# Kernel optimization log

Hardware: AMD Instinct MI355X
Metric: run time of the kernel (lower is better)

Reference implementation:

```python
import jax, jax.numpy as jnp
import numpy as np

D_MODEL = 2048
EXPAND = 2
INNER = EXPAND * D_MODEL          # 4096
HEADDIM = 64
NHEADS = INNER // HEADDIM         # 64
D_CONV = 4
BATCH, SEQLEN = 2, 4096


def setup_inputs() -> dict:
    key = jax.random.key(0)
    ks = jax.random.split(key, 12)
    f32 = jnp.float32
    return {
        "hidden_states": jax.random.normal(ks[0], (BATCH, SEQLEN, D_MODEL), f32),
        "in_proj_w": jax.random.normal(ks[1], (INNER, D_MODEL), f32) * 0.02,
        "gate_proj_w": jax.random.normal(ks[2], (INNER, D_MODEL), f32) * 0.02,
        "out_proj_w": jax.random.normal(ks[3], (D_MODEL, INNER), f32) * 0.02,
        "conv_weight": jax.random.normal(ks[4], (INNER, D_CONV), f32) * 0.02,
        "conv_bias": jnp.zeros((INNER,), f32),
        "dt_w": jax.random.normal(ks[5], (NHEADS, HEADDIM), f32) * 0.02,
        "dt_b": jnp.zeros((NHEADS,), f32),
        "A_log": jax.random.normal(ks[6], (NHEADS, HEADDIM), f32) * 0.1,
        "B": jax.random.normal(ks[7], (NHEADS, HEADDIM), f32) * 0.02,
        "C": jax.random.normal(ks[8], (NHEADS, HEADDIM), f32) * 0.02,
        "D": jnp.ones((NHEADS, HEADDIM), f32),
    }


def _dw_causal_conv_silu(x, w, b):
    # x: (B, L, C), w: (C, K), b: (C,). Causal depthwise conv + SiLU.
    K = w.shape[1]
    L = x.shape[1]
    xp = jnp.pad(x, ((0, 0), (K - 1, 0), (0, 0)))
    y = b
    for k in range(K):  # K=4, tiny fixed loop
        y = y + w[:, k] * xp[:, k:k + L, :]
    return jax.nn.silu(y)


def _diag_ssm_scan(a, u):
    # Linear recurrence s_t = a_t * s_{t-1} + u_t along axis=1 (seqlen).
    def comb(c1, c2):
        a1, b1 = c1
        a2, b2 = c2
        return a1 * a2, a2 * b1 + b2
    _, s = jax.lax.associative_scan(comb, (a, u), axis=1)
    return s


def reference(hidden_states, in_proj_w, gate_proj_w, out_proj_w,
              conv_weight, conv_bias, dt_w, dt_b, A_log, B, C, D):
    batch, seqlen, _ = hidden_states.shape
    projected = jnp.einsum('bld,cd->blc', hidden_states, in_proj_w)
    conv_out = _dw_causal_conv_silu(projected, conv_weight, conv_bias)
    gate = jax.nn.sigmoid(jnp.einsum('bld,cd->blc', hidden_states, gate_proj_w))

    X = conv_out.reshape(batch, seqlen, NHEADS, HEADDIM)
    dt = jax.nn.softplus(jnp.einsum('blhp,hp->blh', X, dt_w) + dt_b)  # (b,l,h)
    A = -jnp.exp(A_log)                                               # (h,p)

    a = jnp.exp(dt[..., None] * A)          # (b,l,h,p) decay factors
    u = dt[..., None] * B * X               # (b,l,h,p) driven input
    s = _diag_ssm_scan(a, u)                # (b,l,h,p) states
    y = C * s + D * X                       # (b,l,h,p)

    combined = y.reshape(batch, seqlen, INNER) * gate
    return jnp.einsum('blc,dc->bld', combined, out_proj_w)
```

## Files before the change

kernel.cpp:

```cpp
#include <hip/hip_runtime.h>
#include <cstdint>
#include <cstddef>

typedef unsigned short ushort;
typedef __attribute__((ext_vector_type(8))) short short8;
typedef __attribute__((ext_vector_type(8))) unsigned short ushort8;
typedef __attribute__((ext_vector_type(4))) float float4v;

#define DM    2048
#define INNERC 4096
#define LSEQ  4096
#define NBATCH 2
#define MROWS 8192
#define NHH   64
#define HDD   64
#define NCHUNK 32
#define CHLEN  128
#define CROWS 8

__device__ __forceinline__ float bf2f(ushort u) {
    return __uint_as_float(((unsigned int)u) << 16);
}
__device__ __forceinline__ ushort f2bf(float f) {
    unsigned int u = __float_as_uint(f);
    unsigned int r = u + 0x7FFFu + ((u >> 16) & 1u);
    return (ushort)(r >> 16);
}

__device__ __forceinline__ void async_cp16(const ushort* __restrict__ g, ushort* l) {
    __builtin_amdgcn_global_load_lds(
        (const __attribute__((address_space(1))) unsigned int*)g,
        (__attribute__((address_space(3))) unsigned int*)l,
        16, 0, 0);
}

__global__ void diag_kernel(float* __restrict__ out, float val) {
    if (threadIdx.x == 0 && blockIdx.x == 0) out[0] = val;
}

__global__ __launch_bounds__(256) void cast_bf16_kernel(
    const float* __restrict__ in, ushort* __restrict__ out, int n) {
    const int i = (blockIdx.x * 256 + threadIdx.x) * 8;
    if (i + 8 > n) return;
    const float4v a = *(const float4v*)(in + i);
    const float4v b = *(const float4v*)(in + i + 4);
    ushort8 o;
    o[0] = f2bf(a[0]); o[1] = f2bf(a[1]); o[2] = f2bf(a[2]); o[3] = f2bf(a[3]);
    o[4] = f2bf(b[0]); o[5] = f2bf(b[1]); o[6] = f2bf(b[2]); o[7] = f2bf(b[3]);
    *(ushort8*)(out + i) = o;
}


#define PHASE_PRE() do { \
    __builtin_amdgcn_sched_barrier(0); \
    __builtin_amdgcn_s_barrier(); \
    asm volatile("s_waitcnt lgkmcnt(0)" ::: "memory"); \
    __builtin_amdgcn_sched_barrier(0); } while (0)

#define PHASE_POST() do { \
    __builtin_amdgcn_sched_barrier(0); \
    __builtin_amdgcn_s_barrier(); } while (0)

#define MFMA_Q(RL, CL) do { \
    __builtin_amdgcn_s_setprio(1); \
    _Pragma("unroll") for (int rm = 0; rm < 4; ++rm) \
    _Pragma("unroll") for (int cn = 0; cn < 2; ++cn) \
    _Pragma("unroll") for (int kk = 0; kk < 2; ++kk) \
        acc[(RL) + rm][(CL) + cn] = __builtin_amdgcn_mfma_f32_16x16x32_bf16( \
            af[(RL) + rm][kk], bf[(CL) + cn][kk], acc[(RL) + rm][(CL) + cn], 0, 0, 0); \
    __builtin_amdgcn_s_setprio(0); } while (0)

#define READ_B2(BUF, CNLO) do { \
    _Pragma("unroll") for (int cn = 0; cn < 2; ++cn) \
    _Pragma("unroll") for (int kk = 0; kk < 2; ++kk) { \
        const int rB = wn * 64 + ((CNLO) + cn) * 16 + l15; \
        bf[(CNLO) + cn][kk] = *(const short8*)&Bs[BUF][ \
            (rB * 8 + ((kk * 4 + l4) ^ swz7)) * 8]; \
    } } while (0)

template <int EPI>
__global__ __launch_bounds__(512, 2) void gemm256(
    const ushort* __restrict__ Ab, const ushort* __restrict__ Wb,
    void* __restrict__ Out, const ushort* __restrict__ Aux,
    int M, int N, int K) {
    __shared__ ushort As[2][16384];
    __shared__ ushort Bs[2][16384];

    const int tid  = threadIdx.x;
    const int lane = tid & 63;
    const int w    = tid >> 6;
    const int wm   = w >> 2;
    const int wn   = w & 3;
    const int l15  = lane & 15;
    const int l4   = lane >> 4;
    const int swz7 = l15 & 7;

    const int gx   = gridDim.x;
    const int nwg  = gx * gridDim.y;
    const int orig = blockIdx.y * gx + blockIdx.x;
    const int swz  = (orig & 7) * (nwg >> 3) + (orig >> 3);
    const int row0 = (swz / gx) * 256;
    const int col0 = (swz % gx) * 256;

    const int ni = K >> 7;

    float4v acc[8][4];
#pragma unroll
    for (int i2 = 0; i2 < 8; i2++)
#pragma unroll
        for (int j2 = 0; j2 < 4; j2++) {
            float4v z = {0.f, 0.f, 0.f, 0.f};
            acc[i2][j2] = z;
        }

    short8 af[8][2], bf[4][2];

    auto stage = [&](const ushort* __restrict__ G, int grow0, int t, ushort* dst) {
#pragma unroll
        for (int j = 0; j < 2; ++j) {
            const int c  = j * 512 + tid;
            const int r  = c >> 3;
            const int kg = (c & 7) ^ (r & 7);
            async_cp16(G + (size_t)(grow0 + r) * K + (t << 6) + kg * 8, dst + c * 8);
        }
    };

    auto readAall = [&](int b) {
#pragma unroll
        for (int rm = 0; rm < 8; ++rm)
#pragma unroll
            for (int kk = 0; kk < 2; ++kk) {
                const int rA = wm * 128 + rm * 16 + l15;
                af[rm][kk] = *(const short8*)&As[b][
                    (rA * 8 + ((kk * 4 + l4) ^ swz7)) * 8];
            }
    };

    stage(Ab, row0,       0, &As[0][0]);
    stage(Ab, row0 + 128, 0, &As[0][8192]);
    stage(Wb, col0,       0, &Bs[0][0]);
    stage(Wb, col0 + 128, 0, &Bs[0][8192]);
    stage(Ab, row0,       1, &As[1][0]);
    stage(Ab, row0 + 128, 1, &As[1][8192]);
    stage(Wb, col0,       1, &Bs[1][0]);
    asm volatile("s_waitcnt vmcnt(6)" ::: "memory");
    __builtin_amdgcn_s_barrier();

#pragma unroll 1
    for (int i = 0; i < ni; ++i) {
        const int u = 2 * i;
        const bool last = (i == ni - 1);

        readAall(0);
        READ_B2(0, 0);
        stage(Wb, col0 + 128, u + 1, &Bs[1][8192]);
        PHASE_PRE();
        MFMA_Q(0, 0);
        PHASE_POST();

        READ_B2(0, 2);
        if (!last) stage(Ab, row0, u + 2, &As[0][0]);
        PHASE_PRE();
        MFMA_Q(0, 2);
        PHASE_POST();

        if (!last) stage(Ab, row0 + 128, u + 2, &As[0][8192]);
        PHASE_PRE();
        MFMA_Q(4, 2);
        PHASE_POST();

        if (!last) stage(Wb, col0, u + 2, &Bs[0][0]);
        PHASE_PRE();
        MFMA_Q(4, 0);
        __builtin_amdgcn_sched_barrier(0);
        if (last) { asm volatile("s_waitcnt vmcnt(0)" ::: "memory"); }
        else      { asm volatile("s_waitcnt vmcnt(6)" ::: "memory"); }
        __builtin_amdgcn_s_barrier();

        readAall(1);
        READ_B2(1, 0);
        if (!last) stage(Wb, col0 + 128, u + 2, &Bs[0][8192]);
        PHASE_PRE();
        MFMA_Q(0, 0);
        PHASE_POST();

        READ_B2(1, 2);
        if (!last) stage(Ab, row0, u + 3, &As[1][0]);
        PHASE_PRE();
        MFMA_Q(0, 2);
        PHASE_POST();

        if (!last) stage(Ab, row0 + 128, u + 3, &As[1][8192]);
        PHASE_PRE();
        MFMA_Q(4, 2);
        PHASE_POST();

        if (!last) stage(Wb, col0, u + 3, &Bs[1][0]);
        PHASE_PRE();
        MFMA_Q(4, 0);
        __builtin_amdgcn_sched_barrier(0);
        if (!last) { asm volatile("s_waitcnt vmcnt(6)" ::: "memory"); }
        __builtin_amdgcn_s_barrier();
    }

#pragma unroll
    for (int rm = 0; rm < 8; ++rm) {
#pragma unroll
        for (int cn = 0; cn < 4; ++cn) {
            const int r0 = row0 + wm * 128 + rm * 16 + l4 * 4;
            const int cc = col0 + wn * 64 + cn * 16 + l15;
#pragma unroll
            for (int rr = 0; rr < 4; ++rr) {
                const float v = acc[rm][cn][rr];
                const size_t off = (size_t)(r0 + rr) * N + cc;
                if (EPI == 0) {
                    ((ushort*)Out)[off] = f2bf(v);
                } else if (EPI == 1) {
                    const float g = 1.0f / (1.0f + __expf(-v));
                    ((ushort*)Out)[off] = f2bf(g * bf2f(Aux[off]));
                } else {
                    ((float*)Out)[off] = v;
                }
            }
        }
    }
}

__global__ __launch_bounds__(256) void conv_silu_kernel(
    const ushort* __restrict__ proj, const float* __restrict__ cw,
    const float* __restrict__ cb, ushort* __restrict__ X) {
    const int blk  = blockIdx.x;
    const int half = blk & 1;
    const int tile = blk >> 1;
    const int bl0  = tile * CROWS;
    const bool atStart = ((bl0 & (LSEQ - 1)) == 0);
    const int c0 = half * 2048 + threadIdx.x * 8;

    float4v w[8];
    const float4v* wp4 = (const float4v*)(cw + (size_t)c0 * 4);
#pragma unroll
    for (int t = 0; t < 8; t++) w[t] = wp4[t];
    float bias[8];
    const float4v b0 = *(const float4v*)(cb + c0);
    const float4v b1 = *(const float4v*)(cb + c0 + 4);
#pragma unroll
    for (int t = 0; t < 4; t++) { bias[t] = b0[t]; bias[t + 4] = b1[t]; }

    const size_t base = (size_t)bl0 * INNERC + c0;
    ushort8 w0, w1, w2;
    const ushort8 zz = {0, 0, 0, 0, 0, 0, 0, 0};
    if (atStart) {
        w0 = zz; w1 = zz; w2 = zz;
    } else {
        w0 = *(const ushort8*)(proj + base - 3 * (size_t)INNERC);
        w1 = *(const ushort8*)(proj + base - 2 * (size_t)INNERC);
        w2 = *(const ushort8*)(proj + base - 1 * (size_t)INNERC);
    }
#pragma unroll
    for (int r = 0; r < CROWS; r++) {
        const ushort8 cur = *(const ushort8*)(proj + base + (size_t)r * INNERC);
        ushort8 o;
#pragma unroll
        for (int j = 0; j < 8; j++) {
            const float acc = bias[j]
                + w[j][0] * bf2f(w0[j]) + w[j][1] * bf2f(w1[j])
                + w[j][2] * bf2f(w2[j]) + w[j][3] * bf2f(cur[j]);
            o[j] = f2bf(acc / (1.0f + __expf(-acc)));
        }
        *(ushort8*)(X + base + (size_t)r * INNERC) = o;
        w0 = w1; w1 = w2; w2 = cur;
    }
}

__global__ __launch_bounds__(64) void dt_kernel(
    const ushort* __restrict__ X, const float* __restrict__ dtw,
    const float* __restrict__ dtb, float* __restrict__ dt) {
    const int bl = blockIdx.x;
    const int h  = threadIdx.x;
    const ushort* xp = X + (size_t)bl * INNERC + h * 64;
    const float*  wp = dtw + h * 64;
    float acc = 0.0f;
#pragma unroll
    for (int p0 = 0; p0 < 64; p0 += 8) {
        const ushort8 xv = *(const ushort8*)(xp + p0);
#pragma unroll
        for (int j = 0; j < 8; j++) acc += bf2f(xv[j]) * wp[p0 + j];
    }
    const float z = acc + dtb[h];
    dt[bl * 64 + h] = (z > 20.0f) ? z : __logf(1.0f + __expf(z));
}

__global__ __launch_bounds__(256) void scan_pass1(
    const ushort* __restrict__ X, const float* __restrict__ dt,
    const float* __restrict__ A_log, const float* __restrict__ Bv,
    float* __restrict__ sumP, float* __restrict__ sumS) {
    const int task = blockIdx.x * 4 + (threadIdx.x >> 6);
    const int p  = threadIdx.x & 63;
    const int ch = task & (NCHUNK - 1);
    const int bh = task >> 5;
    const int h  = bh & 63;
    const int b  = bh >> 6;
    const float Ac = -__expf(A_log[h * 64 + p]);
    const float Bc = Bv[h * 64 + p];
    float Pr = 1.0f, s = 0.0f;
    const int bl0 = b * LSEQ + ch * CHLEN;
#pragma unroll 4
    for (int i = 0; i < CHLEN; i++) {
        const int bl   = bl0 + i;
        const float dtv = dt[bl * 64 + h];
        const float x   = bf2f(X[(size_t)bl * INNERC + h * 64 + p]);
        const float a   = __expf(dtv * Ac);
        Pr *= a;
        s = a * s + dtv * Bc * x;
    }
    sumP[(size_t)task * 64 + p] = Pr;
    sumS[(size_t)task * 64 + p] = s;
}

__global__ __launch_bounds__(64) void scan_pass2(
    const float* __restrict__ sumP, const float* __restrict__ sumS,
    float* __restrict__ carry) {
    const int bh = blockIdx.x;
    const int p  = threadIdx.x;
    float c = 0.0f;
    for (int ch = 0; ch < NCHUNK; ch++) {
        const size_t idx = ((size_t)bh * NCHUNK + ch) * 64 + p;
        carry[idx] = c;
        c = sumP[idx] * c + sumS[idx];
    }
}

__global__ __launch_bounds__(256) void scan_pass3(
    const ushort* __restrict__ X, const float* __restrict__ dt,
    const float* __restrict__ carry,
    const float* __restrict__ A_log, const float* __restrict__ Bv,
    const float* __restrict__ Cv, const float* __restrict__ Dv,
    ushort* __restrict__ Y) {
    const int task = blockIdx.x * 4 + (threadIdx.x >> 6);
    const int p  = threadIdx.x & 63;
    const int ch = task & (NCHUNK - 1);
    const int bh = task >> 5;
    const int h  = bh & 63;
    const int b  = bh >> 6;
    const float Ac = -__expf(A_log[h * 64 + p]);
    const float Bc = Bv[h * 64 + p];
    const float Cc = Cv[h * 64 + p];
    const float Dc = Dv[h * 64 + p];
    float s = carry[(size_t)task * 64 + p];
    const int bl0 = b * LSEQ + ch * CHLEN;
#pragma unroll 2
    for (int i = 0; i < CHLEN; i++) {
        const int bl = bl0 + i;
        const size_t xoff = (size_t)bl * INNERC + h * 64 + p;
        const float dtv = dt[bl * 64 + h];
        const float x   = bf2f(X[xoff]);
        const float a   = __expf(dtv * Ac);
        s = a * s + dtv * Bc * x;
        Y[xoff] = f2bf(Cc * s + Dc * x);
    }
}

#define OFF_PROJ  ((size_t)0)
#define OFF_HID   ((size_t)67108864)
#define OFF_WB    ((size_t)100663296)
#define OFF_DT    ((size_t)117440512)
#define OFF_SUMP  ((size_t)119537664)
#define OFF_SUMS  ((size_t)120586240)
#define OFF_CARRY ((size_t)121634816)
#define WS_NEEDED ((size_t)122683392)

extern "C" void kernel_launch(void* const* d_in, const int* in_sizes, int n_in,
                              void* d_out, int out_size, void* d_ws, size_t ws_size,
                              hipStream_t stream) {
    if (ws_size < WS_NEEDED) {
        diag_kernel<<<1, 64, 0, stream>>>((float*)d_out, (float)(ws_size >> 20));
        return;
    }
    const float* hidden = (const float*)d_in[0];
    const float* w_in   = (const float*)d_in[1];
    const float* w_gate = (const float*)d_in[2];
    const float* w_out  = (const float*)d_in[3];
    const float* conv_w = (const float*)d_in[4];
    const float* conv_b = (const float*)d_in[5];
    const float* dt_w   = (const float*)d_in[6];
    const float* dt_b   = (const float*)d_in[7];
    const float* A_log  = (const float*)d_in[8];
    const float* Bv     = (const float*)d_in[9];
    const float* Cv     = (const float*)d_in[10];
    const float* Dv     = (const float*)d_in[11];

    char* ws = (char*)d_ws;
    ushort* projbuf = (ushort*)(ws + OFF_PROJ);
    ushort* hid16   = (ushort*)(ws + OFF_HID);
    ushort* wbuf    = (ushort*)(ws + OFF_WB);
    float*  dtf     = (float*)(ws + OFF_DT);
    float*  sumP    = (float*)(ws + OFF_SUMP);
    float*  sumS    = (float*)(ws + OFF_SUMS);
    float*  carry   = (float*)(ws + OFF_CARRY);
    ushort* x16     = (ushort*)d_out;

    cast_bf16_kernel<<<8192, 256, 0, stream>>>(hidden, hid16, MROWS * DM);
    cast_bf16_kernel<<<4096, 256, 0, stream>>>(w_in, wbuf, INNERC * DM);

    gemm256<0><<<dim3(INNERC / 256, MROWS / 256), 512, 0, stream>>>(
        hid16, wbuf, projbuf, nullptr, MROWS, INNERC, DM);

    conv_silu_kernel<<<(MROWS / CROWS) * 2, 256, 0, stream>>>(projbuf, conv_w, conv_b, x16);
    dt_kernel<<<MROWS, 64, 0, stream>>>(x16, dt_w, dt_b, dtf);

    scan_pass1<<<(NBATCH * NHH * NCHUNK) / 4, 256, 0, stream>>>(
        x16, dtf, A_log, Bv, sumP, sumS);
    scan_pass2<<<NBATCH * NHH, 64, 0, stream>>>(sumP, sumS, carry);
    scan_pass3<<<(NBATCH * NHH * NCHUNK) / 4, 256, 0, stream>>>(
        x16, dtf, carry, A_log, Bv, Cv, Dv, projbuf);

    cast_bf16_kernel<<<4096, 256, 0, stream>>>(w_gate, wbuf, INNERC * DM);
    gemm256<1><<<dim3(INNERC / 256, MROWS / 256), 512, 0, stream>>>(
        hid16, wbuf, projbuf, projbuf, MROWS, INNERC, DM);

    cast_bf16_kernel<<<4096, 256, 0, stream>>>(w_out, wbuf, DM * INNERC);
    gemm256<2><<<dim3(DM / 256, MROWS / 256), 512, 0, stream>>>(
        projbuf, wbuf, d_out, nullptr, MROWS, DM, INNERC);
}
```

Before: 778.7 us.

## Split A-fragment LDS reads into halves and reorder async staging schedule

Replaces the single 8-row A-fragment register array with two 4-row halves loaded just before their MFMA quadrants, which cuts register pressure and spreads LDS reads across phases. Reorders which global-to-LDS async copies are issued in each phase, prefetching more B in the prologue, and adjusts the vmcnt and lgkmcnt waits to match. It also drops the sched_barrier fences and the memory clobbers on lgkmcnt waits, giving the compiler more freedom to schedule. The risks are hazards from the looser waits and new buffer-reuse ordering (for example, writing As[1] in the same iteration it is read), plus scheduling that is less predictable without the barriers.

New measurement: 683.4 us. -12.2%, faster.

```diff
diff --git a/kernel.cpp b/kernel.cpp
--- a/kernel.cpp
+++ b/kernel.cpp
@@ -51,24 +51,29 @@
 }
 
 
-#define PHASE_PRE() do { \
-    __builtin_amdgcn_sched_barrier(0); \
+#define PH_PRE() do { \
     __builtin_amdgcn_s_barrier(); \
-    asm volatile("s_waitcnt lgkmcnt(0)" ::: "memory"); \
-    __builtin_amdgcn_sched_barrier(0); } while (0)
-
-#define PHASE_POST() do { \
-    __builtin_amdgcn_sched_barrier(0); \
+    asm volatile("s_waitcnt lgkmcnt(0)"); } while (0)
+
+#define PH_POST() do { \
     __builtin_amdgcn_s_barrier(); } while (0)
 
-#define MFMA_Q(RL, CL) do { \
+#define MFMA_Q(AF, RBASE, CL) do { \
     __builtin_amdgcn_s_setprio(1); \
     _Pragma("unroll") for (int rm = 0; rm < 4; ++rm) \
     _Pragma("unroll") for (int cn = 0; cn < 2; ++cn) \
     _Pragma("unroll") for (int kk = 0; kk < 2; ++kk) \
-        acc[(RL) + rm][(CL) + cn] = __builtin_amdgcn_mfma_f32_16x16x32_bf16( \
-            af[(RL) + rm][kk], bf[(CL) + cn][kk], acc[(RL) + rm][(CL) + cn], 0, 0, 0); \
+        acc[(RBASE) + rm][(CL) + cn] = __builtin_amdgcn_mfma_f32_16x16x32_bf16( \
+            AF[rm][kk], bf[(CL) + cn][kk], acc[(RBASE) + rm][(CL) + cn], 0, 0, 0); \
     __builtin_amdgcn_s_setprio(0); } while (0)
+
+#define READ_A(DST, BUF, HB) do { \
+    _Pragma("unroll") for (int rm = 0; rm < 4; ++rm) \
+    _Pragma("unroll") for (int kk = 0; kk < 2; ++kk) { \
+        const int rA = wm * 128 + (HB) * 64 + rm * 16 + l15; \
+        DST[rm][kk] = *(const short8*)&As[BUF][ \
+            (rA * 8 + ((kk * 4 + l4) ^ swz7)) * 8]; \
+    } } while (0)
 
 #define READ_B2(BUF, CNLO) do { \
     _Pragma("unroll") for (int cn = 0; cn < 2; ++cn) \
@@ -113,7 +118,7 @@
             acc[i2][j2] = z;
         }
 
-    short8 af[8][2], bf[4][2];
+    short8 afL[4][2], afH[4][2], bf[4][2];
 
     auto stage = [&](const ushort* __restrict__ G, int grow0, int t, ushort* dst) {
 #pragma unroll
@@ -123,17 +128,6 @@
             const int kg = (c & 7) ^ (r & 7);
             async_cp16(G + (size_t)(grow0 + r) * K + (t << 6) + kg * 8, dst + c * 8);
         }
-    };
-
-    auto readAall = [&](int b) {
-#pragma unroll
-        for (int rm = 0; rm < 8; ++rm)
-#pragma unroll
-            for (int kk = 0; kk < 2; ++kk) {
-                const int rA = wm * 128 + rm * 16 + l15;
-                af[rm][kk] = *(const short8*)&As[b][
-                    (rA * 8 + ((kk * 4 + l4) ^ swz7)) * 8];
-            }
     };
 
     stage(Ab, row0,       0, &As[0][0]);
@@ -143,7 +137,8 @@
     stage(Ab, row0,       1, &As[1][0]);
     stage(Ab, row0 + 128, 1, &As[1][8192]);
     stage(Wb, col0,       1, &Bs[1][0]);
-    asm volatile("s_waitcnt vmcnt(6)" ::: "memory");
+    stage(Wb, col0 + 128, 1, &Bs[1][8192]);
+    asm volatile("s_waitcnt vmcnt(8)" ::: "memory");
     __builtin_amdgcn_s_barrier();
 
 #pragma unroll 1
@@ -151,55 +146,61 @@
         const int u = 2 * i;
         const bool last = (i == ni - 1);
 
-        readAall(0);
+        READ_A(afL, 0, 0);
         READ_B2(0, 0);
-        stage(Wb, col0 + 128, u + 1, &Bs[1][8192]);
-        PHASE_PRE();
-        MFMA_Q(0, 0);
-        PHASE_POST();
+        asm volatile("s_waitcnt lgkmcnt(8)");
+        PH_PRE();
+        MFMA_Q(afL, 0, 0);
+        PH_POST();
 
         READ_B2(0, 2);
+        PH_PRE();
+        MFMA_Q(afL, 0, 2);
+        PH_POST();
+
+        READ_A(afH, 0, 1);
+        if (!last) stage(Wb, col0, u + 2, &Bs[0][0]);
+        PH_PRE();
+        MFMA_Q(afH, 4, 2);
+        PH_POST();
+
+        if (!last) stage(Wb, col0 + 128, u + 2, &Bs[0][8192]);
+        PH_PRE();
+        MFMA_Q(afH, 4, 0);
+        if (last) { asm volatile("s_waitcnt vmcnt(0)" ::: "memory"); }
+        else      { asm volatile("s_waitcnt vmcnt(4)" ::: "memory"); }
+        __builtin_amdgcn_s_barrier();
+
+        READ_A(afL, 1, 0);
+        READ_B2(1, 0);
         if (!last) stage(Ab, row0, u + 2, &As[0][0]);
-        PHASE_PRE();
-        MFMA_Q(0, 2);
-        PHASE_POST();
-
+        asm volatile("s_waitcnt lgkmcnt(8)");
+        PH_PRE();
+        MFMA_Q(afL, 0, 0);
+        PH_POST();
+
+        READ_B2(1, 2);
         if (!last) stage(Ab, row0 + 128, u + 2, &As[0][8192]);
-        PHASE_PRE();
-        MFMA_Q(4, 2);
-        PHASE_POST();
-
-        if (!last) stage(Wb, col0, u + 2, &Bs[0][0]);
-        PHASE_PRE();
-        MFMA_Q(4, 0);
-        __builtin_amdgcn_sched_barrier(0);
-        if (last) { asm volatile("s_waitcnt vmcnt(0)" ::: "memory"); }
-        else      { asm volatile("s_waitcnt vmcnt(6)" ::: "memory"); }
-        __builtin_amdgcn_s_barrier();
-
-        readAall(1);
-        READ_B2(1, 0);
-        if (!last) stage(Wb, col0 + 128, u + 2, &Bs[0][8192]);
-        PHASE_PRE();
-        MFMA_Q(0, 0);
-        PHASE_POST();
-
-        READ_B2(1, 2);
-        if (!last) stage(Ab, row0, u + 3, &As[1][0]);
-        PHASE_PRE();
-        MFMA_Q(0, 2);
-        PHASE_POST();
-
-        if (!last) stage(Ab, row0 + 128, u + 3, &As[1][8192]);
-        PHASE_PRE();
-        MFMA_Q(4, 2);
-        PHASE_POST();
-
-        if (!last) stage(Wb, col0, u + 3, &Bs[1][0]);
-        PHASE_PRE();
-        MFMA_Q(4, 0);
-        __builtin_amdgcn_sched_barrier(0);
-        if (!last) { asm volatile("s_waitcnt vmcnt(6)" ::: "memory"); }
+        PH_PRE();
+        MFMA_Q(afL, 0, 2);
+        PH_POST();
+
+        READ_A(afH, 1, 1);
+        if (!last) {
+            stage(Wb, col0,       u + 3, &Bs[1][0]);
+            stage(Wb, col0 + 128, u + 3, &Bs[1][8192]);
+        }
+        PH_PRE();
+        MFMA_Q(afH, 4, 2);
+        PH_POST();
+
+        if (!last) {
+            stage(Ab, row0,       u + 3, &As[1][0]);
+            stage(Ab, row0 + 128, u + 3, &As[1][8192]);
+        }
+        PH_PRE();
+        MFMA_Q(afH, 4, 0);
+        if (!last) { asm volatile("s_waitcnt vmcnt(8)" ::: "memory"); }
         __builtin_amdgcn_s_barrier();
     }
 
```
